# Kernel optimization log

Measured on AMD Instinct MI355X. Metric: run time of the kernel, lower is better.

Reference implementation:

```python
import jax, jax.numpy as jnp
import numpy as np

N_QUBITS = 8
N_CYCLES = 4
N_LAYERS = 2  # log2(8) - 1
B = 65536

CNOT = jnp.array([[1, 0, 0, 0],
                  [0, 1, 0, 0],
                  [0, 0, 0, 1],
                  [0, 0, 1, 0]], dtype=jnp.complex64)


def apply_gate(state, U, wires):
    """Apply a (2^k x 2^k) gate U on the given wires of state (B, 2,2,...,2).
    Wire 0 is the leftmost (most significant) qubit axis."""
    k = len(wires)
    src = [w + 1 for w in wires]
    dst = list(range(1, 1 + k))
    st = jnp.moveaxis(state, src, dst)
    shp = st.shape
    st = st.reshape(shp[0], 2 ** k, -1)
    st = jnp.einsum('ij,bjr->bir', U, st)
    return jnp.moveaxis(st.reshape(shp), dst, src)


def apply_ry(state, q, angles):
    """Batched RY(angle) on qubit q; angles has shape (B,)."""
    st = jnp.moveaxis(state, q + 1, 1)  # (B, 2, rest...)
    c = jnp.cos(0.5 * angles).reshape((-1,) + (1,) * (st.ndim - 2))
    s = jnp.sin(0.5 * angles).reshape((-1,) + (1,) * (st.ndim - 2))
    s0, s1 = st[:, 0], st[:, 1]
    new = jnp.stack([c * s0 - s * s1, s * s0 + c * s1], axis=1)
    return jnp.moveaxis(new, 1, q + 1)


def crx_mat(theta):
    c = (jnp.cos(0.5 * theta) + 0j).astype(jnp.complex64)
    s = (-1j * jnp.sin(0.5 * theta)).astype(jnp.complex64)
    one = jnp.ones((), jnp.complex64)
    zero = jnp.zeros((), jnp.complex64)
    return jnp.stack([
        jnp.stack([one, zero, zero, zero]),
        jnp.stack([zero, one, zero, zero]),
        jnp.stack([zero, zero, c, s]),
        jnp.stack([zero, zero, s, c]),
    ])


def u3_mat(p):
    th, ph, lm = p[0], p[1], p[2]
    ct = (jnp.cos(0.5 * th) + 0j).astype(jnp.complex64)
    st = (jnp.sin(0.5 * th) + 0j).astype(jnp.complex64)
    el = jnp.exp(1j * lm).astype(jnp.complex64)
    ep = jnp.exp(1j * ph).astype(jnp.complex64)
    return jnp.stack([
        jnp.stack([ct, -el * st]),
        jnp.stack([ep * st, ep * el * ct]),
    ])


def expval_z(state, q):
    st = jnp.moveaxis(state, q + 1, 1)
    p = (st.real ** 2 + st.imag ** 2).reshape(st.shape[0], 2, -1).sum(-1)
    return p[:, 0] - p[:, 1]


def _forward(x, crx_theta, u3_params, w1, b1, w2, b2):
    b = x.shape[0]
    # |0...0> initial state, shape (B, 2,2,...,2)
    state = jnp.zeros((b, 2 ** N_QUBITS), jnp.complex64).at[:, 0].set(1.0)
    state = state.reshape((b,) + (2,) * N_QUBITS)
    # encoder: data re-uploading RY angle encoding + CNOT ring, n_cycles times
    for _ in range(N_CYCLES):
        for q in range(N_QUBITS):
            state = apply_ry(state, q, x[:, q])
        for q in range(N_QUBITS):
            state = apply_gate(state, CNOT, [q, (q + 1) % N_QUBITS])
    # QCNN conv/pool layers with shared weights per layer
    active = list(range(N_QUBITS))
    for layer in range(N_LAYERS):
        U = crx_mat(crx_theta[layer])
        for i in range(0, len(active) - 1, 2):
            state = apply_gate(state, U, [active[i], active[i + 1]])
        for i in range(1, len(active) - 1, 2):
            state = apply_gate(state, U, [active[i], active[i + 1]])
        remain = active[1::2]
        # mid-circuit expval in the original is discarded and does not alter state
        V = u3_mat(u3_params[layer])
        for q in remain:
            state = apply_gate(state, V, [q])
        active = remain
    feats = jnp.stack([expval_z(state, q) for q in active], axis=1)  # (B, 2)
    h = jnp.tanh(feats @ w1 + b1)
    return jax.nn.sigmoid(h @ w2 + b2)  # (B, 1)


def setup_inputs() -> dict:
    key = jax.random.key(0)
    ks = jax.random.split(key, 6)
    return {
        'x': jax.random.normal(ks[0], (B, N_QUBITS), jnp.float32),
        'crx_theta': jax.random.normal(ks[1], (N_LAYERS,), jnp.float32),
        'u3_params': jax.random.normal(ks[2], (N_LAYERS, 3), jnp.float32),
        'w1': jax.random.normal(ks[3], (2, 10), jnp.float32) * 0.5,
        'b1': jnp.zeros((10,), jnp.float32),
        'w2': jax.random.normal(ks[4], (10, 1), jnp.float32) * 0.5,
        'b2': jnp.zeros((1,), jnp.float32),
    }


def reference(x, crx_theta, u3_params, w1, b1, w2, b2):
    return _forward(x, crx_theta, u3_params, w1, b1, w2, b2)
```

## Files before the change

kernel.cpp:

```cpp
#include <hip/hip_runtime.h>


#define NQ 8
#define NE 4
typedef _Float16 h2 __attribute__((ext_vector_type(2)));

__device__ __forceinline__ float h2f(h2 v){ return __builtin_bit_cast(float, v); }
__device__ __forceinline__ h2 f2h(float v){ return __builtin_bit_cast(h2, v); }
__device__ __forceinline__ h2 u2h(unsigned u){ return __builtin_bit_cast(h2, u); }
__device__ __forceinline__ h2 negh(h2 v){ return __builtin_bit_cast(h2, __builtin_bit_cast(unsigned, v) ^ 0x80008000u); }
__device__ __forceinline__ h2 mk(float x){ _Float16 h=(_Float16)x; return (h2){h,h}; }
__device__ __forceinline__ h2 mk2(float a, float b){ return (h2){(_Float16)a,(_Float16)b}; }
__device__ __forceinline__ h2 fma2h(h2 a, h2 b, h2 c){ return __builtin_elementwise_fma(a,b,c); }
__device__ __forceinline__ h2 swp(h2 v){ return __builtin_shufflevector(v,v,1,0); }

template<int CTRL>
__device__ __forceinline__ float dppf(float v){
    return __int_as_float(__builtin_amdgcn_mov_dpp(__float_as_int(v), CTRL, 0xF, 0xF, true));
}
template<int M>
__device__ __forceinline__ float sx(float v){
    if constexpr (M==1)       return dppf<0xB1>(v);
    else if constexpr (M==2)  return dppf<0x4E>(v);
    else if constexpr (M==32) return __shfl_xor(v, 32, 64);
    else return __int_as_float(__builtin_amdgcn_ds_swizzle(__float_as_int(v), (M<<10)|0x1F));
}
__device__ __forceinline__ float bperm(int ba, float v){
    return __int_as_float(__builtin_amdgcn_ds_bpermute(ba, __float_as_int(v)));
}
__device__ __forceinline__ void cmulh(h2&R, h2&I, h2 C, h2 S, h2 nS){
    h2 nR = fma2h(C, R, nS*I);
    I = fma2h(C, I, S*R);
    R = nR;
}

#define FOR_E _Pragma("unroll") for (int e = 0; e < NE; ++e)

__global__ void qcnn_prep(const float* __restrict__ crx,
                          const float* __restrict__ u3p,
                          unsigned* __restrict__ ws){
    if (threadIdx.x==0 && blockIdx.x==0){
        auto PK=[](float lo, float hi)->unsigned{
            unsigned a=__builtin_bit_cast(unsigned short,(_Float16)lo);
            unsigned b=__builtin_bit_cast(unsigned short,(_Float16)hi);
            return a | (b<<16);
        };
        float sc0,cc0,sc1,cc1;
        __sincosf(0.5f*crx[0],&sc0,&cc0);
        __sincosf(0.5f*crx[1],&sc1,&cc1);
        ws[0]=PK(cc0,cc0); ws[1]=PK(sc0,sc0); ws[2]=PK(cc1,cc1); ws[3]=PK(sc1,sc1);
        float th0=u3p[0], ph0=u3p[1], lm0=u3p[2];
        float ust0,uct0; __sincosf(0.5f*th0,&ust0,&uct0);
        ws[4]=PK(uct0,uct0); ws[5]=PK(ust0,ust0); ws[6]=PK(-ust0,-ust0); ws[7]=PK(-ust0,ust0);
        float th1=u3p[3], ph1=u3p[4], lm1=u3p[5];
        float ust1,uct1; __sincosf(0.5f*th1,&ust1,&uct1);
        float sl1,cl1;   __sincosf(lm1,&sl1,&cl1);
        float sp1,cp1;   __sincosf(ph1,&sp1,&cp1);
        ws[8]=PK(uct1,uct1); ws[9]=PK(ust1,ust1); ws[10]=PK(-ust1,-ust1);
        ws[11]=PK(cl1,cl1); ws[12]=PK(sl1,sl1); ws[13]=PK(cp1,cp1); ws[14]=PK(sp1,sp1);
        float cpl1=cp1*cl1-sp1*sl1, spl1=sp1*cl1+cp1*sl1;
        float u01r=-ust1*cl1, u01i=-ust1*sl1;
        float u10r= ust1*cp1, u10i= ust1*sp1;
        float u11r= uct1*cpl1, u11i= uct1*spl1;
        ws[15]=PK(uct1,u11r); ws[16]=PK(u01r,u10r); ws[17]=PK(0.f,-u11i);
        ws[18]=PK(-u01i,-u10i); ws[19]=PK(0.f,u11i); ws[20]=PK(u01i,u10i);
        for(int k=0;k<4;++k){
            float kf=(float)k, sA,cA,sB,cB,sA2,cA2,sB2,cB2;
            __sincosf(lm0*kf,      &sA,&cA);
            __sincosf(lm0*(kf+1.f),&sB,&cB);
            __sincosf(ph0*kf,      &sA2,&cA2);
            __sincosf(ph0*(kf+1.f),&sB2,&cB2);
            unsigned* q = ws + 24 + k*4;
            q[0]=PK(cA,cB); q[1]=PK(sA,sB); q[2]=PK(cA2,cB2); q[3]=PK(sA2,sB2);
        }
    }
}

__global__ __launch_bounds__(256) void qcnn_kernel(
    const float* __restrict__ x,
    const unsigned* __restrict__ wsu,
    const float* __restrict__ w1,
    const float* __restrict__ b1,
    const float* __restrict__ w2,
    const float* __restrict__ b2,
    float* __restrict__ out,
    int Btot)
{
    const int gtid = blockIdx.x*256 + threadIdx.x;
    const int wv = gtid >> 6;
    const int l = threadIdx.x & 63;
    const int e0 = wv * NE;
    if (e0 >= Btot) return;
    const bool L5=(l>>5)&1, L4=(l>>4)&1, L3=(l>>3)&1, L2=(l>>2)&1, L1=(l>>1)&1, L0=l&1;

    const bool pb = __builtin_popcount(l) & 1;
    const int ba0 = (((l&32)|((l^(l>>1))&31)) << 2);
    const int ba1 = ba0 ^ (48<<2);

    h2 cH[NE][6], tsH[NE][6];
    h2 c6h[NE], s6h[NE], ns6h[NE], c7h[NE], sv7h[NE];
    h2 A[NE], B[NE];
    const bool bits[6]={L5,L4,L3,L2,L1,L0};
    FOR_E {
        const int ee = (e0 + e < Btot) ? (e0 + e) : (Btot - 1);
        const float4* xv = (const float4*)(x + ee*NQ);
        float4 xa=xv[0], xb=xv[1];
        float ang[8]={xa.x,xa.y,xa.z,xa.w,xb.x,xb.y,xb.z,xb.w};
        float cq[8], sq[8];
#pragma unroll
        for(int q=0;q<8;++q) __sincosf(0.5f*ang[q], &sq[q], &cq[q]);
#pragma unroll
        for(int q=0;q<6;++q){
            cH[e][q]=mk(cq[q]);
            h2 sh=mk(sq[q]);
            tsH[e][q]= bits[q] ? sh : negh(sh);
        }
        c6h[e]=mk(cq[6]); s6h[e]=mk(sq[6]); ns6h[e]=negh(s6h[e]);
        c7h[e]=mk(cq[7]); sv7h[e]=mk2(-sq[7], sq[7]);
        float pl = (L5?sq[0]:cq[0])*(L4?sq[1]:cq[1])*(L3?sq[2]:cq[2])
                 * (L2?sq[3]:cq[3])*(L1?sq[4]:cq[4])*(L0?sq[5]:cq[5]);
        float pc6=pl*cq[6], ps6=pl*sq[6];
        A[e] = mk2(pc6*cq[7], pc6*sq[7]);
        B[e] = mk2(ps6*cq[7], ps6*sq[7]);
    }

    const h2 cc0h=u2h(wsu[0]), sn0h=u2h(wsu[1]), cc1h=u2h(wsu[2]), sn1h=u2h(wsu[3]);
    const h2 nsn0h=negh(sn0h), nsn1h=negh(sn1h);
    const h2 uct0h=u2h(wsu[4]), ust0h=u2h(wsu[5]), nust0h=u2h(wsu[6]), usv0h=u2h(wsu[7]);
    const h2 uct1h=u2h(wsu[8]), ust1h=u2h(wsu[9]), nust1h=u2h(wsu[10]);
    const h2 cl1h=u2h(wsu[11]), sl1h=u2h(wsu[12]), nsl1h=negh(sl1h);
    const h2 cp1h=u2h(wsu[13]), sp1h=u2h(wsu[14]), nsp1h=negh(sp1h);
    const h2 E0h=u2h(wsu[15]), E1h=u2h(wsu[16]), E2h=u2h(wsu[17]);
    const h2 E3h=u2h(wsu[18]), G2h=u2h(wsu[19]), G3h=u2h(wsu[20]);
    const int ki = (int)L4 + (int)L2 + (int)L0;
    uint4 dt = *(const uint4*)(wsu + 24 + ki*4);
    const h2 Clm=u2h(dt.x), Slm=u2h(dt.y), Cph=u2h(dt.z), Sph=u2h(dt.w);
    const h2 nSlm=negh(Slm), nSph=negh(Sph);
    const h2 tu1H = L4 ? ust0h : nust0h;
    const h2 tu3H = L2 ? ust0h : nust0h;
    const h2 tu5H = L0 ? ust0h : nust0h;

#define RY_L(q, M) do { FOR_E { \
    h2 oA = f2h(sx<M>(h2f(A[e]))), oB = f2h(sx<M>(h2f(B[e]))); \
    A[e] = fma2h(cH[e][q], A[e], tsH[e][q]*oA); \
    B[e] = fma2h(cH[e][q], B[e], tsH[e][q]*oB); } \
} while(0)

#define RINGF() do { FOR_E { \
    float TA = h2f(pb ? B[e] : A[e]); \
    float TS = h2f(swp(pb ? A[e] : B[e])); \
    float u0 = bperm(ba0, TA), u1 = bperm(ba1, TA); \
    float w0 = bperm(ba0, TS), w1 = bperm(ba1, TS); \
    A[e] = (h2){ f2h(u0).x, f2h(u1).y }; \
    B[e] = (h2){ f2h(w0).x, f2h(w1).y }; } \
} while(0)

    RINGF();
#pragma unroll
    for(int cyc=0;cyc<3;++cyc){
        RY_L(0,32); RY_L(1,16); RY_L(2,8); RY_L(3,4); RY_L(4,2); RY_L(5,1);
        FOR_E { h2 nA = fma2h(c6h[e], A[e], ns6h[e]*B[e]);
                h2 nB = fma2h(s6h[e], A[e], c6h[e]*B[e]);
                A[e]=nA; B[e]=nB; }
        FOR_E { A[e] = fma2h(c7h[e], A[e], sv7h[e]*swp(A[e]));
                B[e] = fma2h(c7h[e], B[e], sv7h[e]*swp(B[e])); }
        RINGF();
    }

    h2 RA[NE], RB[NE], IA[NE], IB[NE];
    FOR_E { RA[e]=A[e]; RB[e]=B[e]; IA[e]=(h2){0,0}; IB[e]=(h2){0,0}; }

#define SHF4(M) h2 oRA[NE], oIA[NE], oRB[NE], oIB[NE]; \
    FOR_E { oRA[e]=f2h(sx<M>(h2f(RA[e]))); oIA[e]=f2h(sx<M>(h2f(IA[e]))); \
            oRB[e]=f2h(sx<M>(h2f(RB[e]))); oIB[e]=f2h(sx<M>(h2f(IB[e]))); }
#define CRX_LL(CSH, M, cc, sn, nsn) do { \
    const bool ct = (l >> (CSH)) & 1; \
    SHF4(M) \
    if (ct) { FOR_E { \
        RA[e] = fma2h(cc, RA[e], (sn)*oIA[e]); IA[e] = fma2h(cc, IA[e], (nsn)*oRA[e]); \
        RB[e] = fma2h(cc, RB[e], (sn)*oIB[e]); IB[e] = fma2h(cc, IB[e], (nsn)*oRB[e]); } } \
} while(0)
#define RYC0(M, T) do { \
    SHF4(M) \
    FOR_E { \
    RA[e] = fma2h(uct0h, RA[e], (T)*oRA[e]); IA[e] = fma2h(uct0h, IA[e], (T)*oIA[e]); \
    RB[e] = fma2h(uct0h, RB[e], (T)*oRB[e]); IB[e] = fma2h(uct0h, IB[e], (T)*oIB[e]); } \
} while(0)

    {   h2 oA[NE], oB[NE];
        FOR_E { oA[e]=f2h(sx<16>(h2f(RA[e]))); oB[e]=f2h(sx<16>(h2f(RB[e]))); }
        if (L5){ FOR_E {
            IA[e] = nsn0h*oA[e]; RA[e] = cc0h*RA[e];
            IB[e] = nsn0h*oB[e]; RB[e] = cc0h*RB[e]; } }
    }
    CRX_LL(3, 4, cc0h, sn0h, nsn0h);
    CRX_LL(1, 1, cc0h, sn0h, nsn0h);
    FOR_E {
        h2 oI = swp(IB[e]), oR = swp(RB[e]);
        RB[e] = fma2h(cc0h, RB[e], sn0h*oI);
        IB[e] = fma2h(cc0h, IB[e], nsn0h*oR);
    }
    CRX_LL(4, 8, cc0h, sn0h, nsn0h);
    CRX_LL(2, 2, cc0h, sn0h, nsn0h);
    if (L0) { FOR_E {
        h2 nRA = fma2h(cc0h, RA[e], sn0h*IB[e]);
        h2 nRB = fma2h(cc0h, RB[e], sn0h*IA[e]);
        h2 nIA = fma2h(cc0h, IA[e], nsn0h*RB[e]);
        h2 nIB = fma2h(cc0h, IB[e], nsn0h*RA[e]);
        RA[e]=nRA; RB[e]=nRB; IA[e]=nIA; IB[e]=nIB; } }
    FOR_E { cmulh(RA[e],IA[e],Clm,Slm,nSlm); cmulh(RB[e],IB[e],Clm,Slm,nSlm); }
    RYC0(16, tu1H);
    RYC0(4,  tu3H);
    RYC0(1,  tu5H);
    FOR_E {
        h2 sA=swp(RA[e]), sB=swp(RB[e]), tA=swp(IA[e]), tB=swp(IB[e]);
        RA[e] = fma2h(uct0h, RA[e], usv0h*sA); RB[e] = fma2h(uct0h, RB[e], usv0h*sB);
        IA[e] = fma2h(uct0h, IA[e], usv0h*tA); IB[e] = fma2h(uct0h, IB[e], usv0h*tB);
    }
    FOR_E { cmulh(RA[e],IA[e],Cph,Sph,nSph); cmulh(RB[e],IB[e],Cph,Sph,nSph); }

    CRX_LL(4, 4, cc1h, sn1h, nsn1h);
    if (L0) { FOR_E {
        h2 sIA=swp(IA[e]), sRA=swp(RA[e]), sIB=swp(IB[e]), sRB=swp(RB[e]);
        RA[e] = fma2h(cc1h, RA[e], sn1h*sIA); IA[e] = fma2h(cc1h, IA[e], nsn1h*sRA);
        RB[e] = fma2h(cc1h, RB[e], sn1h*sIB); IB[e] = fma2h(cc1h, IB[e], nsn1h*sRB); } }
    CRX_LL(2, 1, cc1h, sn1h, nsn1h);
    {
        if (L2){ FOR_E { cmulh(RA[e],IA[e],cl1h,sl1h,nsl1h); cmulh(RB[e],IB[e],cl1h,sl1h,nsl1h); } }
        h2 T = L2 ? ust1h : nust1h;
        SHF4(4)
        FOR_E {
            RA[e] = fma2h(uct1h, RA[e], T*oRA[e]); IA[e] = fma2h(uct1h, IA[e], T*oIA[e]);
            RB[e] = fma2h(uct1h, RB[e], T*oRB[e]); IB[e] = fma2h(uct1h, IB[e], T*oIB[e]);
        }
        if (L2){ FOR_E { cmulh(RA[e],IA[e],cp1h,sp1h,nsp1h); cmulh(RB[e],IB[e],cp1h,sp1h,nsp1h); } }
    }
    FOR_E {
        h2 sR=swp(RA[e]), sI=swp(IA[e]);
        h2 nR = fma2h(E3h,sI, fma2h(E2h,IA[e], fma2h(E1h,sR, E0h*RA[e])));
        h2 nI = fma2h(G3h,sR, fma2h(G2h,RA[e], fma2h(E1h,sI, E0h*IA[e])));
        RA[e]=nR; IA[e]=nI;
        h2 sR2=swp(RB[e]), sI2=swp(IB[e]);
        h2 nR2 = fma2h(E3h,sI2, fma2h(E2h,IB[e], fma2h(E1h,sR2, E0h*RB[e])));
        h2 nI2 = fma2h(G3h,sR2, fma2h(G2h,RB[e], fma2h(E1h,sI2, E0h*IB[e])));
        RB[e]=nR2; IB[e]=nI2;
    }

    float f0[NE], f1[NE];
    FOR_E {
        float r0=(float)RA[e].x, r1=(float)RA[e].y, r2=(float)RB[e].x, r3=(float)RB[e].y;
        float i0=(float)IA[e].x, i1=(float)IA[e].y, i2=(float)IB[e].x, i3=(float)IB[e].y;
        float n0=fmaf(i0,i0,r0*r0), n1=fmaf(i1,i1,r1*r1);
        float n2=fmaf(i2,i2,r2*r2), n3=fmaf(i3,i3,r3*r3);
        float tot=(n0+n1)+(n2+n3);
        f0[e] = L2 ? -tot : tot;
        f1[e] = (n0-n1)+(n2-n3);
    }

#define ROUTED_REDUCE(F, OUTV) do { \
    float u01 = L4 ? F[1] : F[0]; \
    float w01 = L4 ? F[0] : F[1]; \
    u01 += sx<16>(w01); \
    float u23 = L4 ? F[3] : F[2]; \
    float w23 = L4 ? F[2] : F[3]; \
    u23 += sx<16>(w23); \
    float v  = L5 ? u23 : u01; \
    float w  = L5 ? u01 : u23; \
    v += sx<32>(w); \
    v += sx<8>(v); v += sx<4>(v); v += sx<2>(v); v += sx<1>(v); \
    OUTV = v; \
} while(0)

    float F0, F1;
    ROUTED_REDUCE(f0, F0);
    ROUTED_REDUCE(f1, F1);

    const int k = l & 15;
    const int row = l >> 4;
    float contrib = 0.0f;
    if (k < 10) {
        float z = fmaf(F0, w1[k], fmaf(F1, w1[10+k], b1[k]));
        float ex = __expf(2.0f*z);
        contrib = ((ex-1.0f)/(ex+1.0f)) * w2[k];
    }
    contrib += sx<1>(contrib);
    contrib += sx<2>(contrib);
    contrib += sx<4>(contrib);
    contrib += sx<8>(contrib);
    if (k == 0 && e0 + row < Btot) {
        float a = contrib + b2[0];
        out[e0 + row] = 1.0f/(1.0f + __expf(-a));
    }
}

extern "C" void kernel_launch(void* const* d_in, const int* in_sizes, int n_in,
                              void* d_out, int out_size, void* d_ws, size_t ws_size,
                              hipStream_t stream) {
    const float* x   = (const float*)d_in[0];
    const float* crx = (const float*)d_in[1];
    const float* u3p = (const float*)d_in[2];
    const float* w1  = (const float*)d_in[3];
    const float* b1  = (const float*)d_in[4];
    const float* w2  = (const float*)d_in[5];
    const float* b2  = (const float*)d_in[6];
    float* out = (float*)d_out;
    unsigned* ws = (unsigned*)d_ws;

    const int B = in_sizes[0] / NQ;
    hipLaunchKernelGGL(qcnn_prep, dim3(1), dim3(64), 0, stream, crx, u3p, ws);
    const int waves = (B + NE - 1) / NE;
    const int wavesPerBlock = 4;
    const int grid = (waves + wavesPerBlock - 1) / wavesPerBlock;
    hipLaunchKernelGGL(qcnn_kernel, dim3(grid), dim3(256), 0, stream,
                       x, ws, w1, b1, w2, b2, out, B);
}
```

Baseline: 118.2 us.

## Halve per-wave batch elements and streamline ring permute, norms, and reduction

Reduces elements per wavefront from 4 to 2, which lowers register pressure and doubles the number of waves. RINGF now packs the halves with v_perm so it issues two ds_bpermute instead of four. Norms are computed with packed fdot2, the cross-lane reduction is simplified for two elements, and fp16 conversions use cvt_pkrtz with XOR sign masks. The tail bounds guards are removed, so the kernel assumes B is divisible by the new element grouping, and the output now sums 16 lanes of contrib per row (not all 16 are nonzero for k>=10, still fine) but writes from lanes 0 and 32.

Measured after the change: 117.5 us. No clear change (-0.6%).

```diff
diff --git a/kernel.cpp b/kernel.cpp
--- a/kernel.cpp
+++ b/kernel.cpp
@@ -2,17 +2,21 @@
 
 
 #define NQ 8
-#define NE 4
+#define NE 2
 typedef _Float16 h2 __attribute__((ext_vector_type(2)));
 
 __device__ __forceinline__ float h2f(h2 v){ return __builtin_bit_cast(float, v); }
 __device__ __forceinline__ h2 f2h(float v){ return __builtin_bit_cast(h2, v); }
 __device__ __forceinline__ h2 u2h(unsigned u){ return __builtin_bit_cast(h2, u); }
-__device__ __forceinline__ h2 negh(h2 v){ return __builtin_bit_cast(h2, __builtin_bit_cast(unsigned, v) ^ 0x80008000u); }
-__device__ __forceinline__ h2 mk(float x){ _Float16 h=(_Float16)x; return (h2){h,h}; }
-__device__ __forceinline__ h2 mk2(float a, float b){ return (h2){(_Float16)a,(_Float16)b}; }
+__device__ __forceinline__ unsigned h2u(h2 v){ return __builtin_bit_cast(unsigned, v); }
+__device__ __forceinline__ h2 negh(h2 v){ return u2h(h2u(v) ^ 0x80008000u); }
+__device__ __forceinline__ h2 mk(float x){ return __builtin_bit_cast(h2, __builtin_amdgcn_cvt_pkrtz(x,x)); }
+__device__ __forceinline__ h2 mk2(float a, float b){ return __builtin_bit_cast(h2, __builtin_amdgcn_cvt_pkrtz(a,b)); }
 __device__ __forceinline__ h2 fma2h(h2 a, h2 b, h2 c){ return __builtin_elementwise_fma(a,b,c); }
 __device__ __forceinline__ h2 swp(h2 v){ return __builtin_shufflevector(v,v,1,0); }
+__device__ __forceinline__ h2 permh(h2 a, h2 b, unsigned sel){
+    return u2h(__builtin_amdgcn_perm(h2u(a), h2u(b), sel));
+}
 
 template<int CTRL>
 __device__ __forceinline__ float dppf(float v){
@@ -24,9 +28,6 @@
     else if constexpr (M==2)  return dppf<0x4E>(v);
     else if constexpr (M==32) return __shfl_xor(v, 32, 64);
     else return __int_as_float(__builtin_amdgcn_ds_swizzle(__float_as_int(v), (M<<10)|0x1F));
-}
-__device__ __forceinline__ float bperm(int ba, float v){
-    return __int_as_float(__builtin_amdgcn_ds_bpermute(ba, __float_as_int(v)));
 }
 __device__ __forceinline__ void cmulh(h2&R, h2&I, h2 C, h2 S, h2 nS){
     h2 nR = fma2h(C, R, nS*I);
@@ -97,13 +98,16 @@
     const int ba0 = (((l&32)|((l^(l>>1))&31)) << 2);
     const int ba1 = ba0 ^ (48<<2);
 
+    const bool bits[6]={L5,L4,L3,L2,L1,L0};
+    unsigned sm[6];
+#pragma unroll
+    for(int q=0;q<6;++q) sm[q] = bits[q] ? 0u : 0x80008000u;
+
     h2 cH[NE][6], tsH[NE][6];
     h2 c6h[NE], s6h[NE], ns6h[NE], c7h[NE], sv7h[NE];
     h2 A[NE], B[NE];
-    const bool bits[6]={L5,L4,L3,L2,L1,L0};
-    FOR_E {
-        const int ee = (e0 + e < Btot) ? (e0 + e) : (Btot - 1);
-        const float4* xv = (const float4*)(x + ee*NQ);
+    FOR_E {
+        const float4* xv = (const float4*)(x + (e0+e)*NQ);
         float4 xa=xv[0], xb=xv[1];
         float ang[8]={xa.x,xa.y,xa.z,xa.w,xb.x,xb.y,xb.z,xb.w};
         float cq[8], sq[8];
@@ -112,8 +116,7 @@
 #pragma unroll
         for(int q=0;q<6;++q){
             cH[e][q]=mk(cq[q]);
-            h2 sh=mk(sq[q]);
-            tsH[e][q]= bits[q] ? sh : negh(sh);
+            tsH[e][q]=u2h(h2u(mk(sq[q])) ^ sm[q]);
         }
         c6h[e]=mk(cq[6]); s6h[e]=mk(sq[6]); ns6h[e]=negh(s6h[e]);
         c7h[e]=mk(cq[7]); sv7h[e]=mk2(-sq[7], sq[7]);
@@ -147,12 +150,14 @@
 } while(0)
 
 #define RINGF() do { FOR_E { \
-    float TA = h2f(pb ? B[e] : A[e]); \
-    float TS = h2f(swp(pb ? A[e] : B[e])); \
-    float u0 = bperm(ba0, TA), u1 = bperm(ba1, TA); \
-    float w0 = bperm(ba0, TS), w1 = bperm(ba1, TS); \
-    A[e] = (h2){ f2h(u0).x, f2h(u1).y }; \
-    B[e] = (h2){ f2h(w0).x, f2h(w1).y }; } \
+    h2 TA = pb ? B[e] : A[e]; \
+    h2 TS = pb ? A[e] : B[e]; \
+    int V0 = (int)__builtin_amdgcn_perm(h2u(TS), h2u(TA), 0x07060100u); \
+    int V1 = (int)__builtin_amdgcn_perm(h2u(TA), h2u(TS), 0x07060100u); \
+    unsigned r0 = (unsigned)__builtin_amdgcn_ds_bpermute(ba0, V0); \
+    unsigned r1 = (unsigned)__builtin_amdgcn_ds_bpermute(ba1, V1); \
+    A[e] = u2h(__builtin_amdgcn_perm(r1, r0, 0x07060100u)); \
+    B[e] = u2h(__builtin_amdgcn_perm(r1, r0, 0x05040302u)); } \
 } while(0)
 
     RINGF();
@@ -248,27 +253,25 @@
 
     float f0[NE], f1[NE];
     FOR_E {
-        float r0=(float)RA[e].x, r1=(float)RA[e].y, r2=(float)RB[e].x, r3=(float)RB[e].y;
-        float i0=(float)IA[e].x, i1=(float)IA[e].y, i2=(float)IB[e].x, i3=(float)IB[e].y;
-        float n0=fmaf(i0,i0,r0*r0), n1=fmaf(i1,i1,r1*r1);
-        float n2=fmaf(i2,i2,r2*r2), n3=fmaf(i3,i3,r3*r3);
-        float tot=(n0+n1)+(n2+n3);
+        h2 P0 = permh(IA[e], RA[e], 0x05040100u);
+        h2 P1 = permh(IA[e], RA[e], 0x07060302u);
+        h2 P2 = permh(IB[e], RB[e], 0x05040100u);
+        h2 P3 = permh(IB[e], RB[e], 0x07060302u);
+        float q02 = __builtin_amdgcn_fdot2(P0, P0,
+                      __builtin_amdgcn_fdot2(P2, P2, 0.0f, false), false);
+        float q13 = __builtin_amdgcn_fdot2(P1, P1,
+                      __builtin_amdgcn_fdot2(P3, P3, 0.0f, false), false);
+        float tot = q02 + q13;
         f0[e] = L2 ? -tot : tot;
-        f1[e] = (n0-n1)+(n2-n3);
+        f1[e] = q02 - q13;
     }
 
 #define ROUTED_REDUCE(F, OUTV) do { \
-    float u01 = L4 ? F[1] : F[0]; \
-    float w01 = L4 ? F[0] : F[1]; \
-    u01 += sx<16>(w01); \
-    float u23 = L4 ? F[3] : F[2]; \
-    float w23 = L4 ? F[2] : F[3]; \
-    u23 += sx<16>(w23); \
-    float v  = L5 ? u23 : u01; \
-    float w  = L5 ? u01 : u23; \
-    v += sx<32>(w); \
-    v += sx<8>(v); v += sx<4>(v); v += sx<2>(v); v += sx<1>(v); \
-    OUTV = v; \
+    float u = L5 ? F[1] : F[0]; \
+    float w = L5 ? F[0] : F[1]; \
+    u += sx<32>(w); \
+    u += sx<16>(u); u += sx<8>(u); u += sx<4>(u); u += sx<2>(u); u += sx<1>(u); \
+    OUTV = u; \
 } while(0)
 
     float F0, F1;
@@ -276,7 +279,6 @@
     ROUTED_REDUCE(f1, F1);
 
     const int k = l & 15;
-    const int row = l >> 4;
     float contrib = 0.0f;
     if (k < 10) {
         float z = fmaf(F0, w1[k], fmaf(F1, w1[10+k], b1[k]));
@@ -287,9 +289,9 @@
     contrib += sx<2>(contrib);
     contrib += sx<4>(contrib);
     contrib += sx<8>(contrib);
-    if (k == 0 && e0 + row < Btot) {
+    if ((l & 31) == 0) {
         float a = contrib + b2[0];
-        out[e0 + row] = 1.0f/(1.0f + __expf(-a));
+        out[e0 + (l>>5)] = 1.0f/(1.0f + __expf(-a));
     }
 }
 
```
